# Kernel tuning notes

Hardware: AMD Instinct MI355X
Metric: run time of the kernel (lower is better)

Reference implementation:

```python
import jax, jax.numpy as jnp
import numpy as np

B, S, H, D = 16, 2048, 768, 128
ATTR_MAX, ITEMS_MAX = 8, 32  # static equivalents of attr_type_ids.max() / item_position_ids max (data generated to hit these)


def setup_inputs() -> dict:
    key = jax.random.key(0)
    k1, k2, k3, k4 = jax.random.split(key, 4)
    return {
        "attention_mask": jnp.ones((B, S), dtype=jnp.int32),
        "hidden_states": jax.random.normal(k1, (B, S, H), dtype=jnp.float32),
        "attr_type_ids": jax.random.randint(k2, (B, S), 0, ATTR_MAX + 1),
        "item_position_ids": jax.random.randint(k3, (B, S), 0, ITEMS_MAX + 1),
        "W": jax.random.normal(k4, (H, D), dtype=jnp.float32) * (1.0 / np.sqrt(H)),
        "b": jnp.zeros((D,), dtype=jnp.float32),
    }


def reference(attention_mask, hidden_states, attr_type_ids, item_position_ids, W, b):
    # linear projection: [B,S,H] @ [H,D] -> [B,S,D]
    h = jnp.einsum('bsh,hd->bsd', hidden_states, W) + b
    Bn, Sn, Dn = h.shape

    # segmented mean over (attr_id, item_id) groups; attr/item id 0 (and >max, e.g. the 50 pad sentinel) are invalid
    valid = (attr_type_ids >= 1) & (attr_type_ids <= ATTR_MAX) & \
            (item_position_ids >= 1) & (item_position_ids <= ITEMS_MAX)
    batch_idx = jnp.arange(Bn)[:, None]
    seg = (batch_idx * ATTR_MAX + (attr_type_ids - 1)) * ITEMS_MAX + (item_position_ids - 1)
    nseg = Bn * ATTR_MAX * ITEMS_MAX
    seg = jnp.where(valid, seg, nseg)  # dump invalid tokens into extra segment
    flat_seg = seg.reshape(-1)

    sums = jax.ops.segment_sum(h.reshape(-1, Dn), flat_seg, num_segments=nseg + 1)[:nseg]
    counts = jax.ops.segment_sum(valid.reshape(-1).astype(h.dtype), flat_seg, num_segments=nseg + 1)[:nseg]

    sums = sums.reshape(Bn, ATTR_MAX, ITEMS_MAX, Dn)
    counts = counts.reshape(Bn, ATTR_MAX, ITEMS_MAX)
    empty = counts == 0
    pooled = sums / jnp.where(empty, jnp.ones_like(counts), counts)[..., None]
    return pooled, empty, h
```

## Files before the change

### kernel.cpp

```cpp
#include <hip/hip_runtime.h>
#include <hip/hip_bf16.h>

#define Bn 16
#define Sn 2048
#define Hn 768
#define Dn 128
#define AT 8
#define IT 32
#define NSEG (Bn*AT*IT)
#define NCHUNK 8
#define CHTOK (Sn/NCHUNK)

typedef __attribute__((ext_vector_type(4))) float f32x4;
typedef __attribute__((ext_vector_type(4))) int   i32x4;
typedef __attribute__((ext_vector_type(8))) short bf16x8;
typedef __attribute__((ext_vector_type(4))) short s16x4;

__device__ __forceinline__ unsigned short f2bf(float f){
  union { float f; unsigned u; } v; v.f = f;
  unsigned r = v.u + 0x7FFFu + ((v.u >> 16) & 1u);
  return (unsigned short)(r >> 16);
}

__global__ __launch_bounds__(256) void k_prep(const float* __restrict__ W,
                                              unsigned short* __restrict__ Wt){
  int gid = blockIdx.x*256 + threadIdx.x;
  if (gid >= Hn*Dn) return;
  int d = gid / Hn;
  int k = gid - d*Hn;
  Wt[gid] = f2bf(W[k*Dn + d]);
}

__global__ __launch_bounds__(256) void k_gemm(const float* __restrict__ X,
        const unsigned short* __restrict__ Wt, const float* __restrict__ bias,
        float* __restrict__ Hout){
  __shared__ unsigned char sA[2][64*128];
  __shared__ unsigned char sB[2][128*128];
  const int tid  = threadIdx.x;
  const int lane = tid & 63;
  const int wave = tid >> 6;
  const int m0 = blockIdx.x * 64;

  const int ar = tid >> 2, akq = tid & 3;
  const int bc = tid >> 1, bkh = tid & 1;
  const float*          Ap = X  + (size_t)(m0 + ar)*Hn + akq*4;
  const unsigned short* Bp = Wt + (size_t)bc*Hn + bkh*32;

  int aw[4], bw[4];
  #pragma unroll
  for (int c=0;c<4;c++) aw[c] = ar*128 + ((akq*8 + c*32) ^ ((ar&7)<<4));
  #pragma unroll
  for (int c=0;c<4;c++) bw[c] = bc*128 + ((bkh*64 + c*16) ^ ((bc&7)<<4));

  int abase[4], aswz[4];
  #pragma unroll
  for (int mi=0;mi<4;mi++){
    int row = mi*16 + (lane&15);
    abase[mi] = row*128; aswz[mi] = (row&7)<<4;
  }
  int bbase[2], bswz[2];
  #pragma unroll
  for (int ni=0;ni<2;ni++){
    int col = wave*32 + ni*16 + (lane&15);
    bbase[ni] = col*128; bswz[ni] = (col&7)<<4;
  }
  const int kblk = (lane>>4)*16;

  f32x4 acc[4][2];
  #pragma unroll
  for (int mi=0;mi<4;mi++)
    #pragma unroll
    for (int ni=0;ni<2;ni++) acc[mi][ni] = (f32x4){0.f,0.f,0.f,0.f};

  f32x4 av[4]; i32x4 bv[4];
  #pragma unroll
  for (int c=0;c<4;c++) av[c] = *(const f32x4*)(Ap + c*16);
  #pragma unroll
  for (int c=0;c<4;c++) bv[c] = *(const i32x4*)(Bp + c*8);
  #pragma unroll
  for (int c=0;c<4;c++){
    s16x4 t;
    t[0]=(short)f2bf(av[c][0]); t[1]=(short)f2bf(av[c][1]);
    t[2]=(short)f2bf(av[c][2]); t[3]=(short)f2bf(av[c][3]);
    *(s16x4*)&sA[0][aw[c]] = t;
  }
  #pragma unroll
  for (int c=0;c<4;c++) *(i32x4*)&sB[0][bw[c]] = bv[c];
  __syncthreads();

  int cur = 0;
  for (int step=0; step<12; ++step){
    if (step < 11){
      #pragma unroll
      for (int c=0;c<4;c++) av[c] = *(const f32x4*)(Ap + (step+1)*64 + c*16);
      #pragma unroll
      for (int c=0;c<4;c++) bv[c] = *(const i32x4*)(Bp + (step+1)*64 + c*8);
    }
    #pragma unroll
    for (int ks=0; ks<2; ++ks){
      bf16x8 af[4], bfv[2];
      #pragma unroll
      for (int mi=0;mi<4;mi++)
        af[mi] = *(const bf16x8*)&sA[cur][abase[mi] + ((ks*64 + kblk) ^ aswz[mi])];
      #pragma unroll
      for (int ni=0;ni<2;ni++)
        bfv[ni] = *(const bf16x8*)&sB[cur][bbase[ni] + ((ks*64 + kblk) ^ bswz[ni])];
      #pragma unroll
      for (int mi=0;mi<4;mi++)
        #pragma unroll
        for (int ni=0;ni<2;ni++)
          acc[mi][ni] = __builtin_amdgcn_mfma_f32_16x16x32_bf16(af[mi], bfv[ni], acc[mi][ni], 0, 0, 0);
    }
    if (step < 11){
      #pragma unroll
      for (int c=0;c<4;c++){
        s16x4 t;
        t[0]=(short)f2bf(av[c][0]); t[1]=(short)f2bf(av[c][1]);
        t[2]=(short)f2bf(av[c][2]); t[3]=(short)f2bf(av[c][3]);
        *(s16x4*)&sA[cur^1][aw[c]] = t;
      }
      #pragma unroll
      for (int c=0;c<4;c++) *(i32x4*)&sB[cur^1][bw[c]] = bv[c];
    }
    __syncthreads();
    cur ^= 1;
  }

  #pragma unroll
  for (int ni=0;ni<2;ni++){
    int col = wave*32 + ni*16 + (lane&15);
    float bb = bias[col];
    #pragma unroll
    for (int mi=0;mi<4;mi++){
      int row0 = m0 + mi*16 + (lane>>4)*4;
      #pragma unroll
      for (int r=0;r<4;r++)
        Hout[(size_t)(row0 + r)*Dn + col] = acc[mi][ni][r] + bb;
    }
  }
}

__global__ __launch_bounds__(128) void k_scan(const int* __restrict__ attr,
        const int* __restrict__ item, const float* __restrict__ Hsrc,
        float* __restrict__ psums, float* __restrict__ pcnts){
  __shared__ float ssum[IT][Dn];
  __shared__ int   scnt[IT];
  __shared__ int   slist[CHTOK];

  const int wg  = blockIdx.x;
  const int c   = wg & (NCHUNK-1);
  const int a   = (wg / NCHUNK) & 7;
  const int b   = wg / (NCHUNK*AT);
  const int tid = threadIdx.x;
  const int lane = tid & 63;

  for (int i = tid; i < IT*Dn; i += 128) (&ssum[0][0])[i] = 0.f;
  if (tid < IT) scnt[tid] = 0;

  const int tglob0 = b*Sn + c*CHTOK;
  int base = 0;
  #pragma unroll
  for (int g=0; g<CHTOK/64; ++g){
    int t = tglob0 + g*64 + lane;
    int avv = attr[t], ivv = item[t];
    bool m = (avv == a+1) && (ivv >= 1) && (ivv <= IT);
    unsigned long long mask = __ballot(m);
    int pos = base + __popcll(mask & ((1ull<<lane)-1ull));
    if (m) slist[pos] = ((ivv-1) << 16) | (c*CHTOK + g*64 + lane);
    base += __popcll(mask);
  }
  const int nm = base;
  __syncthreads();

  for (int e = tid; e < nm; e += 128) atomicAdd(&scnt[slist[e] >> 16], 1);

  const float* hb = Hsrc + (size_t)b*Sn*Dn;
  int e = 0;
  for (; e + 4 <= nm; e += 4){
    int p0=slist[e], p1=slist[e+1], p2=slist[e+2], p3=slist[e+3];
    float v0 = hb[(p0 & 0xffff)*Dn + tid];
    float v1 = hb[(p1 & 0xffff)*Dn + tid];
    float v2 = hb[(p2 & 0xffff)*Dn + tid];
    float v3 = hb[(p3 & 0xffff)*Dn + tid];
    ssum[p0>>16][tid] += v0;
    ssum[p1>>16][tid] += v1;
    ssum[p2>>16][tid] += v2;
    ssum[p3>>16][tid] += v3;
  }
  for (; e < nm; ++e){
    int p = slist[e];
    ssum[p>>16][tid] += hb[(p & 0xffff)*Dn + tid];
  }
  __syncthreads();

  float* outp = psums + (size_t)wg*IT*Dn;
  for (int i=0;i<IT;i++) outp[i*Dn + tid] = ssum[i][tid];
  if (tid < IT) pcnts[wg*IT + tid] = (float)scnt[tid];
}

__global__ __launch_bounds__(256) void k_comb(const float* __restrict__ psums,
        const float* __restrict__ pcnts, float* __restrict__ pooled,
        float* __restrict__ empty){
  int gid = blockIdx.x*256 + threadIdx.x;
  int seg = gid >> 7;
  int d   = gid & 127;
  int ba  = seg >> 5;
  int i   = seg & 31;
  float s = 0.f, cnt = 0.f;
  #pragma unroll
  for (int cch=0; cch<NCHUNK; ++cch){
    int wg = ba*NCHUNK + cch;
    s   += psums[(size_t)wg*IT*Dn + i*Dn + d];
    cnt += pcnts[wg*IT + i];
  }
  float div = cnt > 0.f ? cnt : 1.f;
  pooled[gid] = s / div;
  if (d == 0) empty[seg] = (cnt == 0.f) ? 1.f : 0.f;
}

extern "C" void kernel_launch(void* const* d_in, const int* in_sizes, int n_in,
                              void* d_out, int out_size, void* d_ws, size_t ws_size,
                              hipStream_t stream) {
  const float* hidden = (const float*)d_in[1];
  const int*   attr   = (const int*)  d_in[2];
  const int*   item   = (const int*)  d_in[3];
  const float* W      = (const float*)d_in[4];
  const float* bias   = (const float*)d_in[5];

  float* pooled = (float*)d_out;
  float* empty  = pooled + (size_t)NSEG*Dn;
  float* Hout   = empty  + NSEG;

  unsigned short* Wt = (unsigned short*)d_ws;
  float* psums = (float*)((char*)d_ws + 196608);
  float* pcnts = psums + (size_t)Bn*AT*NCHUNK*IT*Dn;

  k_prep<<<(Hn*Dn + 255)/256, 256, 0, stream>>>(W, Wt);
  k_gemm<<<(Bn*Sn)/64, 256, 0, stream>>>(hidden, Wt, bias, Hout);
  k_scan<<<Bn*AT*NCHUNK, 128, 0, stream>>>(attr, item, Hout, psums, pcnts);
  k_comb<<<(NSEG*Dn)/256, 256, 0, stream>>>(psums, pcnts, pooled, empty);
}
```

Before: 43.45 us.

## Fuse segment scan and combine into one kernel with per-wave shared accumulators

Replaces the chunked scan kernel and the separate combine kernel with a single kernel that has one workgroup per (batch, attr). Each of its four waves scans a quarter of the sequence into its own shared-memory partial sums, and the partials are reduced and divided in shared memory. This removes the partial-sum workspace round trip and one kernel launch. It also gathers H rows as float2 per lane and unrolls the gather by 8. In exchange the grid shrinks from 1024 to 128 workgroups, and the larger shared-memory footprint (about 72KB) lowers occupancy.

```diff
diff --git a/kernel.cpp b/kernel.cpp
--- a/kernel.cpp
+++ b/kernel.cpp
@@ -8,10 +8,9 @@
 #define AT 8
 #define IT 32
 #define NSEG (Bn*AT*IT)
-#define NCHUNK 8
-#define CHTOK (Sn/NCHUNK)
 
 typedef __attribute__((ext_vector_type(4))) float f32x4;
+typedef __attribute__((ext_vector_type(2))) float f32x2;
 typedef __attribute__((ext_vector_type(4))) int   i32x4;
 typedef __attribute__((ext_vector_type(8))) short bf16x8;
 typedef __attribute__((ext_vector_type(4))) short s16x4;
@@ -140,82 +139,72 @@
   }
 }
 
-__global__ __launch_bounds__(128) void k_scan(const int* __restrict__ attr,
+__global__ __launch_bounds__(256) void k_scan(const int* __restrict__ attr,
         const int* __restrict__ item, const float* __restrict__ Hsrc,
-        float* __restrict__ psums, float* __restrict__ pcnts){
-  __shared__ float ssum[IT][Dn];
+        float* __restrict__ pooled, float* __restrict__ empty){
+  __shared__ float ssum[4][IT][Dn];
+  __shared__ int   slist[4][512];
   __shared__ int   scnt[IT];
-  __shared__ int   slist[CHTOK];
 
   const int wg  = blockIdx.x;
-  const int c   = wg & (NCHUNK-1);
-  const int a   = (wg / NCHUNK) & 7;
-  const int b   = wg / (NCHUNK*AT);
+  const int a   = wg & 7;
+  const int b   = wg >> 3;
   const int tid = threadIdx.x;
+  const int wv  = tid >> 6;
   const int lane = tid & 63;
 
-  for (int i = tid; i < IT*Dn; i += 128) (&ssum[0][0])[i] = 0.f;
+  for (int i = tid; i < 4*IT*Dn; i += 256) (&ssum[0][0][0])[i] = 0.f;
   if (tid < IT) scnt[tid] = 0;
-
-  const int tglob0 = b*Sn + c*CHTOK;
-  int base = 0;
-  #pragma unroll
-  for (int g=0; g<CHTOK/64; ++g){
-    int t = tglob0 + g*64 + lane;
-    int avv = attr[t], ivv = item[t];
+  __syncthreads();
+
+  const int tok0 = wv * 512;
+  const int gbase = b * Sn;
+  int nm = 0;
+  #pragma unroll
+  for (int g = 0; g < 8; ++g){
+    int tok = tok0 + g*64 + lane;
+    int avv = attr[gbase + tok], ivv = item[gbase + tok];
     bool m = (avv == a+1) && (ivv >= 1) && (ivv <= IT);
     unsigned long long mask = __ballot(m);
-    int pos = base + __popcll(mask & ((1ull<<lane)-1ull));
-    if (m) slist[pos] = ((ivv-1) << 16) | (c*CHTOK + g*64 + lane);
-    base += __popcll(mask);
-  }
-  const int nm = base;
+    int pos = nm + __popcll(mask & ((1ull << lane) - 1ull));
+    if (m){
+      slist[wv][pos] = ((ivv-1) << 16) | tok;
+      atomicAdd(&scnt[ivv-1], 1);
+    }
+    nm += __popcll(mask);
+  }
+
+  const f32x2* hb = (const f32x2*)(Hsrc + (size_t)b*Sn*Dn);
+  float* myacc = &ssum[wv][0][0];
+  int e = 0;
+  for (; e + 8 <= nm; e += 8){
+    int idx[8]; f32x2 v[8];
+    #pragma unroll
+    for (int j=0;j<8;j++) idx[j] = slist[wv][e+j];
+    #pragma unroll
+    for (int j=0;j<8;j++) v[j] = hb[(size_t)(idx[j] & 0xffff)*64 + lane];
+    #pragma unroll
+    for (int j=0;j<8;j++){
+      f32x2* p = (f32x2*)&myacc[(idx[j]>>16)*Dn + lane*2];
+      f32x2 old = *p; old[0] += v[j][0]; old[1] += v[j][1]; *p = old;
+    }
+  }
+  for (; e < nm; ++e){
+    int idx = slist[wv][e];
+    f32x2 v = hb[(size_t)(idx & 0xffff)*64 + lane];
+    f32x2* p = (f32x2*)&myacc[(idx>>16)*Dn + lane*2];
+    f32x2 old = *p; old[0] += v[0]; old[1] += v[1]; *p = old;
+  }
   __syncthreads();
 
-  for (int e = tid; e < nm; e += 128) atomicAdd(&scnt[slist[e] >> 16], 1);
-
-  const float* hb = Hsrc + (size_t)b*Sn*Dn;
-  int e = 0;
-  for (; e + 4 <= nm; e += 4){
-    int p0=slist[e], p1=slist[e+1], p2=slist[e+2], p3=slist[e+3];
-    float v0 = hb[(p0 & 0xffff)*Dn + tid];
-    float v1 = hb[(p1 & 0xffff)*Dn + tid];
-    float v2 = hb[(p2 & 0xffff)*Dn + tid];
-    float v3 = hb[(p3 & 0xffff)*Dn + tid];
-    ssum[p0>>16][tid] += v0;
-    ssum[p1>>16][tid] += v1;
-    ssum[p2>>16][tid] += v2;
-    ssum[p3>>16][tid] += v3;
-  }
-  for (; e < nm; ++e){
-    int p = slist[e];
-    ssum[p>>16][tid] += hb[(p & 0xffff)*Dn + tid];
-  }
-  __syncthreads();
-
-  float* outp = psums + (size_t)wg*IT*Dn;
-  for (int i=0;i<IT;i++) outp[i*Dn + tid] = ssum[i][tid];
-  if (tid < IT) pcnts[wg*IT + tid] = (float)scnt[tid];
-}
-
-__global__ __launch_bounds__(256) void k_comb(const float* __restrict__ psums,
-        const float* __restrict__ pcnts, float* __restrict__ pooled,
-        float* __restrict__ empty){
-  int gid = blockIdx.x*256 + threadIdx.x;
-  int seg = gid >> 7;
-  int d   = gid & 127;
-  int ba  = seg >> 5;
-  int i   = seg & 31;
-  float s = 0.f, cnt = 0.f;
-  #pragma unroll
-  for (int cch=0; cch<NCHUNK; ++cch){
-    int wg = ba*NCHUNK + cch;
-    s   += psums[(size_t)wg*IT*Dn + i*Dn + d];
-    cnt += pcnts[wg*IT + i];
-  }
-  float div = cnt > 0.f ? cnt : 1.f;
-  pooled[gid] = s / div;
-  if (d == 0) empty[seg] = (cnt == 0.f) ? 1.f : 0.f;
+  float* outp = pooled + (size_t)wg*IT*Dn;
+  for (int o = tid; o < IT*Dn; o += 256){
+    int i = o >> 7, d = o & 127;
+    float s = ssum[0][i][d] + ssum[1][i][d] + ssum[2][i][d] + ssum[3][i][d];
+    int cnt = scnt[i];
+    outp[o] = s / (float)(cnt > 0 ? cnt : 1);
+  }
+  if (tid < IT) empty[wg*IT + tid] = (scnt[tid] == 0) ? 1.f : 0.f;
 }
 
 extern "C" void kernel_launch(void* const* d_in, const int* in_sizes, int n_in,
@@ -232,11 +221,8 @@
   float* Hout   = empty  + NSEG;
 
   unsigned short* Wt = (unsigned short*)d_ws;
-  float* psums = (float*)((char*)d_ws + 196608);
-  float* pcnts = psums + (size_t)Bn*AT*NCHUNK*IT*Dn;
 
   k_prep<<<(Hn*Dn + 255)/256, 256, 0, stream>>>(W, Wt);
   k_gemm<<<(Bn*Sn)/64, 256, 0, stream>>>(hidden, Wt, bias, Hout);
-  k_scan<<<Bn*AT*NCHUNK, 128, 0, stream>>>(attr, item, Hout, psums, pcnts);
-  k_comb<<<(NSEG*Dn)/256, 256, 0, stream>>>(psums, pcnts, pooled, empty);
-}
+  k_scan<<<Bn*AT, 256, 0, stream>>>(attr, item, Hout, pooled, empty);
+}
```

Measured after the change: 42.27 us. 2.7% less time.
